# Performance work log

Measured on AMD Instinct MI355X. Metric: run time of the kernel, lower is better.

The kernel has to match this reference:

```python
import jax, jax.numpy as jnp
import numpy as np

T, D_IN, D_OUT = 8192, 1024, 1024
TRACE, CONTEXT = 64, 16


def setup_inputs() -> dict:
    key = jax.random.key(0)
    ks = jax.random.split(key, 8)
    x = jax.random.normal(ks[0], (T, D_IN), jnp.float32)
    state_re = jnp.zeros((1, TRACE, CONTEXT), jnp.float32)
    state_im = jnp.zeros((1, TRACE, CONTEXT), jnp.float32)
    start = jax.random.bernoulli(ks[1], 0.01, (T,))
    next_done = jax.random.bernoulli(ks[2], 0.01, (T,))
    lim_in = 1.0 / np.sqrt(D_IN)
    W_pre = jax.random.uniform(ks[3], (TRACE, D_IN), jnp.float32, -lim_in, lim_in)
    b_pre = jnp.zeros((TRACE,), jnp.float32)
    W_skip = jax.random.uniform(ks[4], (D_OUT, D_IN), jnp.float32, -lim_in, lim_in)
    b_skip = jnp.zeros((D_OUT,), jnp.float32)
    d_mix = 2 * TRACE * CONTEXT
    lim_mix = 1.0 / np.sqrt(d_mix)
    W_mix = jax.random.uniform(ks[5], (D_OUT, d_mix), jnp.float32, -lim_mix, lim_mix)
    b_mix = jnp.zeros((D_OUT,), jnp.float32)
    # ffa.init: deterministic decay rates a and oscillation freqs b (FFM paper)
    a = jnp.linspace(1e-6, 0.5, TRACE)
    b_freq = 2.0 * jnp.pi / jnp.linspace(1.0, 1024.0, CONTEXT)
    return dict(x=x, state_re=state_re, state_im=state_im, start=start, next_done=next_done,
                W_pre=W_pre, b_pre=b_pre, W_skip=W_skip, b_skip=b_skip,
                W_mix=W_mix, b_mix=b_mix, a=a, b_freq=b_freq)


def _ffa_scan(pre, state0, start, a, b_freq):
    """Resettable complex linear recurrence: S_t = gamma * S_{t-1} * !start_t + pre_t.
    pre: [T, m] real, state0: [1, m, c] complex. Returns [T, m, c] complex."""
    n = pre.shape[0]
    ab = (-jnp.abs(a)[:, None] + 1j * b_freq[None, :]).astype(jnp.complex64)  # [m, c]
    x_c = jnp.broadcast_to(pre[:, :, None], (n, pre.shape[1], b_freq.shape[0])).astype(jnp.complex64)
    # prepend carried-in state as an extra element with no decay (t=0) and no reset
    x_c = jnp.concatenate([state0, x_c], axis=0)
    s = jnp.concatenate([jnp.zeros((1,), bool), start.astype(bool)], axis=0)
    t = jnp.concatenate([jnp.zeros((1,), jnp.float32), jnp.ones((n,), jnp.float32)], axis=0)

    def combine(l, r):
        sl, xl, tl = l
        sr, xr, tr = r
        keep = jnp.logical_not(sr)  # right segment starts an episode -> drop left
        decay = jnp.exp(ab[None, :, :] * tr[:, None, None])  # gamma^{t_right}
        x = jnp.where(keep[:, None, None], xl * decay, jnp.zeros((), jnp.complex64)) + xr
        return (jnp.logical_or(sl, sr), x, tl * keep + tr)

    _, states, _ = jax.lax.associative_scan(combine, (s, x_c, t), axis=0)
    return states[1:]


def reference(x, state_re, state_im, start, next_done,
              W_pre, b_pre, W_skip, b_skip, W_mix, b_mix, a, b_freq):
    pre = x @ W_pre.T + b_pre                                  # [T, m]
    pre = pre / (1e-6 + jnp.linalg.norm(pre, axis=-1, keepdims=True))
    state0 = (state_re + 1j * state_im).astype(jnp.complex64)   # [1, m, c]
    states = _ffa_scan(pre, state0, start, a, b_freq)           # [T, m, c] complex
    z_in = jnp.concatenate([jnp.real(states), jnp.imag(states)], axis=-1)
    z_in = z_in.reshape(states.shape[0], -1)                    # [T, 2*m*c]
    z = z_in @ W_mix.T + b_mix                                  # [T, d_out]
    skip = x @ W_skip.T + b_skip                                # [T, d_out]
    return (z + skip, states[-1:])
```

## Files before the change

kernel.cpp:

```cpp
#include <hip/hip_runtime.h>
#include <hip/hip_bf16.h>
#include <stdint.h>

#define T_LEN 8192
#define DIN   1024
#define DOUT  1024
#define TRACE 64
#define CTX   16
#define KTOT  3072
#define CH    64
#define NCHUNK 128

#define AS1 __attribute__((address_space(1)))
#define AS3 __attribute__((address_space(3)))

#define BAR() asm volatile("s_barrier" ::: "memory")

using bf16 = __hip_bfloat16;
typedef __attribute__((ext_vector_type(4))) float f32x4;
typedef __attribute__((ext_vector_type(8))) short s16x8;

__device__ __forceinline__ void pack4(const float4 v, void* dst) {
    union { bf16 h[4]; uint2 u; } pk;
    pk.h[0] = __float2bfloat16(v.x); pk.h[1] = __float2bfloat16(v.y);
    pk.h[2] = __float2bfloat16(v.z); pk.h[3] = __float2bfloat16(v.w);
    *(uint2*)dst = pk.u;
}

__global__ void cvt_all(const float* __restrict__ x, const float* __restrict__ Wsk,
                        const float* __restrict__ Wmx, const float* __restrict__ Wpre,
                        bf16* __restrict__ A, bf16* __restrict__ Bc, bf16* __restrict__ Wp) {
    int idx = blockIdx.x * 256 + threadIdx.x;
    if (idx < 2097152) {
        int r = idx >> 8, c4 = (idx & 255) << 2;
        pack4(*(const float4*)(x + (size_t)r * 1024 + c4), A + (size_t)r * KTOT + c4);
    } else if (idx < 2359296) {
        int i = idx - 2097152;
        int r = i >> 8, c4 = (i & 255) << 2;
        pack4(*(const float4*)(Wsk + (size_t)r * 1024 + c4), Bc + (size_t)r * KTOT + c4);
    } else if (idx < 2883584) {
        int i = idx - 2359296;
        int r = i >> 9, c4 = (i & 511) << 2;
        pack4(*(const float4*)(Wmx + (size_t)r * 2048 + c4), Bc + (size_t)r * KTOT + 1024 + c4);
    } else if (idx < 2899968) {
        int i = idx - 2883584;
        int r = i >> 8, c4 = (i & 255) << 2;
        pack4(*(const float4*)(Wpre + (size_t)r * 1024 + c4), Wp + (size_t)r * 1024 + c4);
    }
}

__global__ __launch_bounds__(256) void pre_scan1(
    const bf16* __restrict__ A,
    const bf16* __restrict__ Wp,
    const float* __restrict__ bpre,
    const int* __restrict__ start,
    const float* __restrict__ a, const float* __restrict__ bfreq,
    float* __restrict__ pre_raw,
    float2* __restrict__ local_end,
    int* __restrict__ reset_any) {
    __shared__ short As[2][64 * 32];
    __shared__ short Bs[2][64 * 32];
    __shared__ float pn[CH][TRACE + 1];
    __shared__ float rn[CH];
    __shared__ int sf[CH];
    const int tid = threadIdx.x, lane = tid & 63, wv = tid >> 6;
    const int row0 = blockIdx.x * 64;
    const int l4 = lane >> 2, c8 = (lane & 3) * 8;

    auto stage = [&](int kt, int buf) {
        int r = wv * 16 + l4;
        const bf16* ga = A + (size_t)(row0 + r) * KTOT + kt * 32 + c8;
        const bf16* gb = Wp + (size_t)r * 1024 + kt * 32 + c8;
        __builtin_amdgcn_global_load_lds(
            (const AS1 void*)ga, (AS3 void*)&As[buf][wv * 512], 16, 0, 0);
        __builtin_amdgcn_global_load_lds(
            (const AS1 void*)gb, (AS3 void*)&Bs[buf][wv * 512], 16, 0, 0);
    };

    f32x4 acc[4];
#pragma unroll
    for (int j = 0; j < 4; ++j) acc[j] = (f32x4)0.0f;

    stage(0, 0);
    __syncthreads();
    int buf = 0;
    const int lr = lane & 15, lk = (lane >> 4) * 8;
    for (int kt = 0; kt < 32; ++kt) {
        if (kt + 1 < 32) stage(kt + 1, buf ^ 1);
        s16x8 af = *(const s16x8*)&As[buf][(wv * 16 + lr) * 32 + lk];
        s16x8 bfr[4];
#pragma unroll
        for (int j = 0; j < 4; ++j)
            bfr[j] = *(const s16x8*)&Bs[buf][(j * 16 + lr) * 32 + lk];
#pragma unroll
        for (int j = 0; j < 4; ++j)
            acc[j] = __builtin_amdgcn_mfma_f32_16x16x32_bf16(af, bfr[j], acc[j], 0, 0, 0);
        __syncthreads();
        buf ^= 1;
    }
    const int lg = lane >> 4;
#pragma unroll
    for (int j = 0; j < 4; ++j) {
        int col = j * 16 + lr;
        float bias = bpre[col];
#pragma unroll
        for (int r = 0; r < 4; ++r) {
            int rl = wv * 16 + lg * 4 + r;
            float v = acc[j][r] + bias;
            pn[rl][col] = v;
            pre_raw[(size_t)(row0 + rl) * TRACE + col] = v;
        }
    }
    if (tid < CH) sf[tid] = start[row0 + tid];
    __syncthreads();
    if (tid < CH) {
        float s = 0.f;
#pragma unroll
        for (int m = 0; m < TRACE; ++m) { float v = pn[tid][m]; s += v * v; }
        rn[tid] = 1.0f / (1e-6f + sqrtf(s));
        int any = __any(sf[tid] != 0);
        if (tid == 0) reset_any[blockIdx.x] = any;
    }
    __syncthreads();
#pragma unroll
    for (int q = 0; q < 4; ++q) {
        int pair = tid + q * 256;
        int m = pair >> 4, c = pair & 15;
        float am = a[m], th = bfreq[c];
        float e = expf(-fabsf(am));
        float sn, cs; sincosf(th, &sn, &cs);
        float gr = e * cs, gi = e * sn;
        float sre = 0.f, sim = 0.f;
        for (int r = 0; r < CH; ++r) {
            float p = pn[r][m] * rn[r];
            if (sf[r]) { sre = p; sim = 0.f; }
            else { float t = gr * sre - gi * sim + p; sim = gr * sim + gi * sre; sre = t; }
        }
        local_end[(size_t)blockIdx.x * 1024 + pair] = make_float2(sre, sim);
    }
}

__global__ void scan_phase2(const float2* __restrict__ local_end, const int* __restrict__ reset_any,
                            const float* __restrict__ state_re, const float* __restrict__ state_im,
                            const float* __restrict__ a, const float* __restrict__ bfreq,
                            float2* __restrict__ carry_in, float* __restrict__ out_tail, int tail_n) {
    const int pair = blockIdx.x * 64 + threadIdx.x;
    const int m = pair >> 4, c = pair & 15;
    float am = a[m], th = bfreq[c];
    float e = expf(-64.f * fabsf(am));
    float sn, cs; sincosf(64.f * th, &sn, &cs);
    float gr = e * cs, gi = e * sn;
    float cre = state_re[pair], cim = state_im[pair];

    float2 pf[8]; int rsv[8];
#pragma unroll
    for (int j = 0; j < 8; ++j) { pf[j] = local_end[(size_t)j * 1024 + pair]; rsv[j] = reset_any[j]; }
    for (int kb = 0; kb < NCHUNK; kb += 8) {
        float2 cur[8]; int rs[8];
#pragma unroll
        for (int j = 0; j < 8; ++j) { cur[j] = pf[j]; rs[j] = rsv[j]; }
        if (kb + 8 < NCHUNK) {
#pragma unroll
            for (int j = 0; j < 8; ++j) {
                pf[j]  = local_end[(size_t)(kb + 8 + j) * 1024 + pair];
                rsv[j] = reset_any[kb + 8 + j];
            }
        }
#pragma unroll
        for (int j = 0; j < 8; ++j) {
            carry_in[(size_t)(kb + j) * 1024 + pair] = make_float2(cre, cim);
            if (rs[j]) { cre = cur[j].x; cim = cur[j].y; }
            else {
                float t = gr * cre - gi * cim + cur[j].x;
                cim = gr * cim + gi * cre + cur[j].y;
                cre = t;
            }
        }
    }
    if (pair < tail_n)        out_tail[pair]        = cre;
    if (1024 + pair < tail_n) out_tail[1024 + pair] = cim;
}

__global__ void scan_phase3(const float* __restrict__ pre_raw, const int* __restrict__ start,
                            const float* __restrict__ a, const float* __restrict__ bfreq,
                            const float2* __restrict__ carry_in, bf16* __restrict__ A) {
    __shared__ float pn[CH][TRACE + 1];
    __shared__ float rn[CH];
    __shared__ int sf[CH];
    const int k = blockIdx.x, tid = threadIdx.x;
    for (int idx = tid; idx < CH * TRACE; idx += 256) {
        int r = idx >> 6, m = idx & 63;
        pn[r][m] = pre_raw[(size_t)(k * CH + r) * TRACE + m];
    }
    if (tid < CH) sf[tid] = start[k * CH + tid];
    __syncthreads();
    if (tid < CH) {
        float s = 0.f;
#pragma unroll
        for (int m = 0; m < TRACE; ++m) { float v = pn[tid][m]; s += v * v; }
        rn[tid] = 1.0f / (1e-6f + sqrtf(s));
    }
    __syncthreads();
#pragma unroll
    for (int q = 0; q < 2; ++q) {
        int p0 = q * 512 + tid * 2;
        int m = p0 >> 4, c0 = p0 & 15;
        float am = a[m];
        float e = expf(-fabsf(am));
        float sn0, cs0, sn1, cs1;
        sincosf(bfreq[c0], &sn0, &cs0);
        sincosf(bfreq[c0 + 1], &sn1, &cs1);
        float gr0 = e * cs0, gi0 = e * sn0;
        float gr1 = e * cs1, gi1 = e * sn1;
        float4 ci = *(const float4*)&carry_in[(size_t)k * 1024 + p0];
        float sre0 = ci.x, sim0 = ci.y, sre1 = ci.z, sim1 = ci.w;
        for (int r = 0; r < CH; ++r) {
            float p = pn[r][m] * rn[r];
            if (sf[r]) { sre0 = p; sim0 = 0.f; sre1 = p; sim1 = 0.f; }
            else {
                float t0 = gr0 * sre0 - gi0 * sim0 + p; sim0 = gr0 * sim0 + gi0 * sre0; sre0 = t0;
                float t1 = gr1 * sre1 - gi1 * sim1 + p; sim1 = gr1 * sim1 + gi1 * sre1; sre1 = t1;
            }
            size_t off = (size_t)(k * CH + r) * KTOT + 1024 + m * 32;
            union { bf16 h[2]; uint32_t u; } pr, pi;
            pr.h[0] = __float2bfloat16(sre0); pr.h[1] = __float2bfloat16(sre1);
            pi.h[0] = __float2bfloat16(sim0); pi.h[1] = __float2bfloat16(sim1);
            *(uint32_t*)(A + off + c0)      = pr.u;
            *(uint32_t*)(A + off + 16 + c0) = pi.u;
        }
    }
}

__global__ __launch_bounds__(512) void gemm_main(const bf16* __restrict__ A,
                                                 const bf16* __restrict__ B,
                                                 const float* __restrict__ bskip,
                                                 const float* __restrict__ bmix,
                                                 float* __restrict__ out) {
    __shared__ short As[3][256 * 64];
    __shared__ short Bs[3][128 * 64];
    const int tid = threadIdx.x;
    const int lane = tid & 63, wv = tid >> 6;
    const int wm = wv >> 1, wn = wv & 1;
    const int wg = blockIdx.x;
    const int xcd = wg & 7, bidx = wg >> 3;
    const int row0 = (xcd * 4 + (bidx >> 3)) * 256;
    const int col0 = (bidx & 7) * 128;

    const int rl8 = lane >> 3;
    const int u8  = lane & 7;
    const int ksw = (u8 ^ rl8) << 3;

    auto stageBatch = [&](int su, int bd, int sb) {
#pragma unroll
        for (int jj = 0; jj < 2; ++jj) {
            int j = sb * 2 + jj;
            int r = wv * 32 + j * 8 + rl8;
            const bf16* ga = A + (size_t)(row0 + r) * KTOT + su * 64 + ksw;
            __builtin_amdgcn_global_load_lds((const AS1 void*)ga,
                (AS3 void*)&As[bd][(wv * 32 + j * 8) * 64], 16, 0, 0);
        }
        int rb = wv * 16 + sb * 8 + rl8;
        const bf16* gb = B + (size_t)(col0 + rb) * KTOT + su * 64 + ksw;
        __builtin_amdgcn_global_load_lds((const AS1 void*)gb,
            (AS3 void*)&Bs[bd][(wv * 16 + sb * 8) * 64], 16, 0, 0);
    };

    f32x4 acc[4][4];
#pragma unroll
    for (int i = 0; i < 4; ++i)
#pragma unroll
        for (int j = 0; j < 4; ++j) acc[i][j] = (f32x4)0.0f;

    const int lr = lane & 15, hi = lane >> 4;
    const int sw0 = ((0 + hi) ^ (lr & 7)) << 3;
    const int sw1 = ((4 + hi) ^ (lr & 7)) << 3;

    s16x8 af[4][2], bfr[4][2];

    auto phase = [&](int bc, int h, int su, int bd, int vm) {
        if (h == 0) {
#pragma unroll
            for (int i = 0; i < 4; ++i) {
                af[i][0] = *(const s16x8*)&As[bc][(wm * 64 + i * 16 + lr) * 64 + sw0];
                af[i][1] = *(const s16x8*)&As[bc][(wm * 64 + i * 16 + lr) * 64 + sw1];
            }
#pragma unroll
            for (int j = 0; j < 2; ++j) {
                bfr[j][0] = *(const s16x8*)&Bs[bc][(wn * 64 + j * 16 + lr) * 64 + sw0];
                bfr[j][1] = *(const s16x8*)&Bs[bc][(wn * 64 + j * 16 + lr) * 64 + sw1];
            }
        } else {
#pragma unroll
            for (int j = 2; j < 4; ++j) {
                bfr[j][0] = *(const s16x8*)&Bs[bc][(wn * 64 + j * 16 + lr) * 64 + sw0];
                bfr[j][1] = *(const s16x8*)&Bs[bc][(wn * 64 + j * 16 + lr) * 64 + sw1];
            }
        }
        if (su >= 0) stageBatch(su, bd, h);
        BAR();
        __builtin_amdgcn_s_setprio(1);
#pragma unroll
        for (int kk = 0; kk < 2; ++kk)
#pragma unroll
            for (int i = 0; i < 4; ++i)
#pragma unroll
                for (int jj = 0; jj < 2; ++jj) {
                    int j = h * 2 + jj;
                    acc[i][j] = __builtin_amdgcn_mfma_f32_16x16x32_bf16(af[i][kk], bfr[j][kk], acc[i][j], 0, 0, 0);
                }
        __builtin_amdgcn_s_setprio(0);
        if (vm == 6)      asm volatile("s_waitcnt vmcnt(6)" ::: "memory");
        else if (vm == 0) asm volatile("s_waitcnt vmcnt(0)" ::: "memory");
        asm volatile("s_waitcnt lgkmcnt(0)" ::: "memory");
        BAR();
    };

    stageBatch(0, 0, 0); stageBatch(0, 0, 1);
    stageBatch(1, 1, 0); stageBatch(1, 1, 1);
    asm volatile("s_waitcnt vmcnt(6)" ::: "memory");
    BAR();

    for (int t = 0; t < 15; ++t) {
        int u0 = 3 * t;
        phase(0, 0, u0 + 2, 2, -1);
        phase(0, 1, u0 + 2, 2,  6);
        phase(1, 0, u0 + 3, 0, -1);
        phase(1, 1, u0 + 3, 0,  6);
        phase(2, 0, u0 + 4, 1, -1);
        phase(2, 1, u0 + 4, 1,  6);
    }
    phase(0, 0, 47, 2, -1);
    phase(0, 1, 47, 2,  6);
    phase(1, 0, -1, 0, -1);
    phase(1, 1, -1, 0,  0);
    phase(2, 0, -1, 0, -1);
    phase(2, 1, -1, 0, -1);

    const int lg = lane >> 4;
#pragma unroll
    for (int j = 0; j < 4; ++j) {
        int col = col0 + wn * 64 + j * 16 + lr;
        float bias = bskip[col] + bmix[col];
#pragma unroll
        for (int i = 0; i < 4; ++i) {
            int rbase = row0 + wm * 64 + i * 16 + lg * 4;
#pragma unroll
            for (int r = 0; r < 4; ++r)
                out[(size_t)(rbase + r) * DOUT + col] = acc[i][j][r] + bias;
        }
    }
}

extern "C" void kernel_launch(void* const* d_in, const int* in_sizes, int n_in,
                              void* d_out, int out_size, void* d_ws, size_t ws_size,
                              hipStream_t stream) {
    const float* x        = (const float*)d_in[0];
    const float* state_re = (const float*)d_in[1];
    const float* state_im = (const float*)d_in[2];
    const int*   start    = (const int*)d_in[3];
    const float* W_pre    = (const float*)d_in[5];
    const float* b_pre    = (const float*)d_in[6];
    const float* W_skip   = (const float*)d_in[7];
    const float* b_skip   = (const float*)d_in[8];
    const float* W_mix    = (const float*)d_in[9];
    const float* b_mix    = (const float*)d_in[10];
    const float* a_dec    = (const float*)d_in[11];
    const float* b_freq   = (const float*)d_in[12];

    uint8_t* ws = (uint8_t*)d_ws;
    bf16*  A         = (bf16*)(ws);
    bf16*  Bc        = (bf16*)(ws + 50331648);
    bf16*  Wp        = (bf16*)(ws + 56623104);
    float* pre_raw   = (float*)(ws + 56754176);
    float2* local_end= (float2*)(ws + 58851328);
    float2* carry_in = (float2*)(ws + 59899904);
    int*   reset_any = (int*)(ws + 60948480);

    cvt_all<<<dim3((2899968 + 255) / 256), 256, 0, stream>>>(x, W_skip, W_mix, W_pre, A, Bc, Wp);

    pre_scan1<<<dim3(NCHUNK), 256, 0, stream>>>(A, Wp, b_pre, start, a_dec, b_freq,
                                                pre_raw, local_end, reset_any);
    int tail_n = out_size - 8192 * 1024;
    if (tail_n < 0) tail_n = 0;
    if (tail_n > 2048) tail_n = 2048;
    scan_phase2<<<dim3(16), 64, 0, stream>>>(local_end, reset_any, state_re, state_im, a_dec, b_freq,
                                             carry_in, (float*)d_out + 8192 * 1024, tail_n);
    scan_phase3<<<dim3(NCHUNK), 256, 0, stream>>>(pre_raw, start, a_dec, b_freq, carry_in, A);

    gemm_main<<<dim3(256), 512, 0, stream>>>(A, Bc, b_skip, b_mix, (float*)d_out);
}
```

Baseline: 124.2 us.

## Split scan phase3 into half-size chunks using mid-chunk carries

Pre-scan now also records each 64-row chunk's local state at row 32, plus per-half reset flags. Phase2 uses these to derive carry-ins at 32-row granularity, applying a 32-step decay for the mid point. Phase3 then launches twice as many blocks, each with a 32-step sequential recurrence, to shorten its serial latency and raise occupancy. The cost is extra local_mid traffic and more work in the single-pass phase2.

```diff
diff --git a/kernel.cpp b/kernel.cpp
--- a/kernel.cpp
+++ b/kernel.cpp
@@ -9,7 +9,9 @@
 #define CTX   16
 #define KTOT  3072
 #define CH    64
+#define CH2   32
 #define NCHUNK 128
+#define NCHUNK2 256
 
 #define AS1 __attribute__((address_space(1)))
 #define AS3 __attribute__((address_space(3)))
@@ -57,7 +59,8 @@
     const float* __restrict__ a, const float* __restrict__ bfreq,
     float* __restrict__ pre_raw,
     float2* __restrict__ local_end,
-    int* __restrict__ reset_any) {
+    float2* __restrict__ local_mid,
+    int* __restrict__ ra0, int* __restrict__ ra1) {
     __shared__ short As[2][64 * 32];
     __shared__ short Bs[2][64 * 32];
     __shared__ float pn[CH][TRACE + 1];
@@ -118,8 +121,11 @@
 #pragma unroll
         for (int m = 0; m < TRACE; ++m) { float v = pn[tid][m]; s += v * v; }
         rn[tid] = 1.0f / (1e-6f + sqrtf(s));
-        int any = __any(sf[tid] != 0);
-        if (tid == 0) reset_any[blockIdx.x] = any;
+        unsigned long long b = __ballot(sf[tid] != 0);
+        if (tid == 0) {
+            ra0[blockIdx.x] = (b & 0xffffffffull) != 0;
+            ra1[blockIdx.x] = (b >> 32) != 0;
+        }
     }
     __syncthreads();
 #pragma unroll
@@ -135,44 +141,64 @@
             float p = pn[r][m] * rn[r];
             if (sf[r]) { sre = p; sim = 0.f; }
             else { float t = gr * sre - gi * sim + p; sim = gr * sim + gi * sre; sre = t; }
+            if (r == CH2 - 1)
+                local_mid[(size_t)blockIdx.x * 1024 + pair] = make_float2(sre, sim);
         }
         local_end[(size_t)blockIdx.x * 1024 + pair] = make_float2(sre, sim);
     }
 }
 
-__global__ void scan_phase2(const float2* __restrict__ local_end, const int* __restrict__ reset_any,
+__global__ void scan_phase2(const float2* __restrict__ local_end, const float2* __restrict__ local_mid,
+                            const int* __restrict__ ra0, const int* __restrict__ ra1,
                             const float* __restrict__ state_re, const float* __restrict__ state_im,
                             const float* __restrict__ a, const float* __restrict__ bfreq,
-                            float2* __restrict__ carry_in, float* __restrict__ out_tail, int tail_n) {
+                            float2* __restrict__ carry_in,
+                            float* __restrict__ out_tail, int tail_n) {
     const int pair = blockIdx.x * 64 + threadIdx.x;
     const int m = pair >> 4, c = pair & 15;
     float am = a[m], th = bfreq[c];
-    float e = expf(-64.f * fabsf(am));
-    float sn, cs; sincosf(64.f * th, &sn, &cs);
-    float gr = e * cs, gi = e * sn;
+    float e64 = expf(-64.f * fabsf(am));
+    float sn64, cs64; sincosf(64.f * th, &sn64, &cs64);
+    float gr64 = e64 * cs64, gi64 = e64 * sn64;
+    float e32 = expf(-32.f * fabsf(am));
+    float sn32, cs32; sincosf(32.f * th, &sn32, &cs32);
+    float gr32 = e32 * cs32, gi32 = e32 * sn32;
     float cre = state_re[pair], cim = state_im[pair];
 
-    float2 pf[8]; int rsv[8];
-#pragma unroll
-    for (int j = 0; j < 8; ++j) { pf[j] = local_end[(size_t)j * 1024 + pair]; rsv[j] = reset_any[j]; }
+    float2 pfE[8], pfM[8]; int pf0[8], pf1[8];
+#pragma unroll
+    for (int j = 0; j < 8; ++j) {
+        pfE[j] = local_end[(size_t)j * 1024 + pair];
+        pfM[j] = local_mid[(size_t)j * 1024 + pair];
+        pf0[j] = ra0[j]; pf1[j] = ra1[j];
+    }
     for (int kb = 0; kb < NCHUNK; kb += 8) {
-        float2 cur[8]; int rs[8];
-#pragma unroll
-        for (int j = 0; j < 8; ++j) { cur[j] = pf[j]; rs[j] = rsv[j]; }
+        float2 curE[8], curM[8]; int r0[8], r1[8];
+#pragma unroll
+        for (int j = 0; j < 8; ++j) { curE[j] = pfE[j]; curM[j] = pfM[j]; r0[j] = pf0[j]; r1[j] = pf1[j]; }
         if (kb + 8 < NCHUNK) {
 #pragma unroll
             for (int j = 0; j < 8; ++j) {
-                pf[j]  = local_end[(size_t)(kb + 8 + j) * 1024 + pair];
-                rsv[j] = reset_any[kb + 8 + j];
+                pfE[j] = local_end[(size_t)(kb + 8 + j) * 1024 + pair];
+                pfM[j] = local_mid[(size_t)(kb + 8 + j) * 1024 + pair];
+                pf0[j] = ra0[kb + 8 + j]; pf1[j] = ra1[kb + 8 + j];
             }
         }
 #pragma unroll
         for (int j = 0; j < 8; ++j) {
-            carry_in[(size_t)(kb + j) * 1024 + pair] = make_float2(cre, cim);
-            if (rs[j]) { cre = cur[j].x; cim = cur[j].y; }
+            int k = kb + j;
+            carry_in[(size_t)(2 * k) * 1024 + pair] = make_float2(cre, cim);
+            float hre, him;
+            if (r0[j]) { hre = curM[j].x; him = curM[j].y; }
             else {
-                float t = gr * cre - gi * cim + cur[j].x;
-                cim = gr * cim + gi * cre + cur[j].y;
+                hre = gr32 * cre - gi32 * cim + curM[j].x;
+                him = gr32 * cim + gi32 * cre + curM[j].y;
+            }
+            carry_in[(size_t)(2 * k + 1) * 1024 + pair] = make_float2(hre, him);
+            if (r0[j] | r1[j]) { cre = curE[j].x; cim = curE[j].y; }
+            else {
+                float t = gr64 * cre - gi64 * cim + curE[j].x;
+                cim = gr64 * cim + gi64 * cre + curE[j].y;
                 cre = t;
             }
         }
@@ -184,17 +210,18 @@
 __global__ void scan_phase3(const float* __restrict__ pre_raw, const int* __restrict__ start,
                             const float* __restrict__ a, const float* __restrict__ bfreq,
                             const float2* __restrict__ carry_in, bf16* __restrict__ A) {
-    __shared__ float pn[CH][TRACE + 1];
-    __shared__ float rn[CH];
-    __shared__ int sf[CH];
+    __shared__ float pn[CH2][TRACE + 1];
+    __shared__ float rn[CH2];
+    __shared__ int sf[CH2];
     const int k = blockIdx.x, tid = threadIdx.x;
-    for (int idx = tid; idx < CH * TRACE; idx += 256) {
+    const int rowb = k * CH2;
+    for (int idx = tid; idx < CH2 * TRACE; idx += 256) {
         int r = idx >> 6, m = idx & 63;
-        pn[r][m] = pre_raw[(size_t)(k * CH + r) * TRACE + m];
-    }
-    if (tid < CH) sf[tid] = start[k * CH + tid];
+        pn[r][m] = pre_raw[(size_t)(rowb + r) * TRACE + m];
+    }
+    if (tid < CH2) sf[tid] = start[rowb + tid];
     __syncthreads();
-    if (tid < CH) {
+    if (tid < CH2) {
         float s = 0.f;
 #pragma unroll
         for (int m = 0; m < TRACE; ++m) { float v = pn[tid][m]; s += v * v; }
@@ -214,14 +241,14 @@
         float gr1 = e * cs1, gi1 = e * sn1;
         float4 ci = *(const float4*)&carry_in[(size_t)k * 1024 + p0];
         float sre0 = ci.x, sim0 = ci.y, sre1 = ci.z, sim1 = ci.w;
-        for (int r = 0; r < CH; ++r) {
+        for (int r = 0; r < CH2; ++r) {
             float p = pn[r][m] * rn[r];
             if (sf[r]) { sre0 = p; sim0 = 0.f; sre1 = p; sim1 = 0.f; }
             else {
                 float t0 = gr0 * sre0 - gi0 * sim0 + p; sim0 = gr0 * sim0 + gi0 * sre0; sre0 = t0;
                 float t1 = gr1 * sre1 - gi1 * sim1 + p; sim1 = gr1 * sim1 + gi1 * sre1; sre1 = t1;
             }
-            size_t off = (size_t)(k * CH + r) * KTOT + 1024 + m * 32;
+            size_t off = (size_t)(rowb + r) * KTOT + 1024 + m * 32;
             union { bf16 h[2]; uint32_t u; } pr, pi;
             pr.h[0] = __float2bfloat16(sre0); pr.h[1] = __float2bfloat16(sre1);
             pi.h[0] = __float2bfloat16(sim0); pi.h[1] = __float2bfloat16(sim1);
@@ -373,19 +400,22 @@
     bf16*  Wp        = (bf16*)(ws + 56623104);
     float* pre_raw   = (float*)(ws + 56754176);
     float2* local_end= (float2*)(ws + 58851328);
-    float2* carry_in = (float2*)(ws + 59899904);
-    int*   reset_any = (int*)(ws + 60948480);
+    float2* local_mid= (float2*)(ws + 59899904);
+    float2* carry_in = (float2*)(ws + 60948480);
+    int*   ra0       = (int*)(ws + 63045632);
+    int*   ra1       = (int*)(ws + 63046656);
 
     cvt_all<<<dim3((2899968 + 255) / 256), 256, 0, stream>>>(x, W_skip, W_mix, W_pre, A, Bc, Wp);
 
     pre_scan1<<<dim3(NCHUNK), 256, 0, stream>>>(A, Wp, b_pre, start, a_dec, b_freq,
-                                                pre_raw, local_end, reset_any);
+                                                pre_raw, local_end, local_mid, ra0, ra1);
     int tail_n = out_size - 8192 * 1024;
     if (tail_n < 0) tail_n = 0;
     if (tail_n > 2048) tail_n = 2048;
-    scan_phase2<<<dim3(16), 64, 0, stream>>>(local_end, reset_any, state_re, state_im, a_dec, b_freq,
+    scan_phase2<<<dim3(16), 64, 0, stream>>>(local_end, local_mid, ra0, ra1,
+                                             state_re, state_im, a_dec, b_freq,
                                              carry_in, (float*)d_out + 8192 * 1024, tail_n);
-    scan_phase3<<<dim3(NCHUNK), 256, 0, stream>>>(pre_raw, start, a_dec, b_freq, carry_in, A);
+    scan_phase3<<<dim3(NCHUNK2), 256, 0, stream>>>(pre_raw, start, a_dec, b_freq, carry_in, A);
 
     gemm_main<<<dim3(256), 512, 0, stream>>>(A, Bc, b_skip, b_mix, (float*)d_out);
 }
```

Result: slower. 129.4 us (+4.2%).

## Fuse x bf16 conversion into pre-GEMM and overlap weight conversion with scan phase 2

Applied to the files above, without the earlier changes.

The x-to-bf16 conversion moves into pre_scan1, which loads fp32 x rows, packs them to bf16, writes them both to LDS for the MFMA and to the A buffer for the main GEMM. W_pre is now preloaded whole into LDS once per block. The W_skip/W_mix conversion is folded into the tiny scan_phase2 launch as extra blocks so it runs alongside the serial carry scan. This drops a separate pass over x and hides the weight conversion behind a latency-bound kernel, at the cost of a larger LDS footprint and extra barriers in pre_scan1.

```diff
diff --git a/kernel.cpp b/kernel.cpp
--- a/kernel.cpp
+++ b/kernel.cpp
@@ -10,6 +10,7 @@
 #define KTOT  3072
 #define CH    64
 #define NCHUNK 128
+#define WPLD  1032
 
 #define AS1 __attribute__((address_space(1)))
 #define AS3 __attribute__((address_space(3)))
@@ -27,75 +28,88 @@
     *(uint2*)dst = pk.u;
 }
 
-__global__ void cvt_all(const float* __restrict__ x, const float* __restrict__ Wsk,
-                        const float* __restrict__ Wmx, const float* __restrict__ Wpre,
-                        bf16* __restrict__ A, bf16* __restrict__ Bc, bf16* __restrict__ Wp) {
+__device__ __forceinline__ uint4 pack8(const float4 a, const float4 b) {
+    union { bf16 h[8]; uint4 u; } pk;
+    pk.h[0] = __float2bfloat16(a.x); pk.h[1] = __float2bfloat16(a.y);
+    pk.h[2] = __float2bfloat16(a.z); pk.h[3] = __float2bfloat16(a.w);
+    pk.h[4] = __float2bfloat16(b.x); pk.h[5] = __float2bfloat16(b.y);
+    pk.h[6] = __float2bfloat16(b.z); pk.h[7] = __float2bfloat16(b.w);
+    return pk.u;
+}
+
+__global__ void cvt_wp(const float* __restrict__ Wpre, bf16* __restrict__ Wp) {
     int idx = blockIdx.x * 256 + threadIdx.x;
-    if (idx < 2097152) {
-        int r = idx >> 8, c4 = (idx & 255) << 2;
-        pack4(*(const float4*)(x + (size_t)r * 1024 + c4), A + (size_t)r * KTOT + c4);
-    } else if (idx < 2359296) {
-        int i = idx - 2097152;
-        int r = i >> 8, c4 = (i & 255) << 2;
-        pack4(*(const float4*)(Wsk + (size_t)r * 1024 + c4), Bc + (size_t)r * KTOT + c4);
-    } else if (idx < 2883584) {
-        int i = idx - 2359296;
-        int r = i >> 9, c4 = (i & 511) << 2;
-        pack4(*(const float4*)(Wmx + (size_t)r * 2048 + c4), Bc + (size_t)r * KTOT + 1024 + c4);
-    } else if (idx < 2899968) {
-        int i = idx - 2883584;
-        int r = i >> 8, c4 = (i & 255) << 2;
-        pack4(*(const float4*)(Wpre + (size_t)r * 1024 + c4), Wp + (size_t)r * 1024 + c4);
-    }
+    int r = idx >> 8, c4 = (idx & 255) << 2;
+    pack4(*(const float4*)(Wpre + (size_t)r * 1024 + c4), Wp + (size_t)r * 1024 + c4);
 }
 
 __global__ __launch_bounds__(256) void pre_scan1(
-    const bf16* __restrict__ A,
+    const float* __restrict__ x,
     const bf16* __restrict__ Wp,
+    bf16* __restrict__ A,
     const float* __restrict__ bpre,
     const int* __restrict__ start,
     const float* __restrict__ a, const float* __restrict__ bfreq,
     float* __restrict__ pre_raw,
     float2* __restrict__ local_end,
     int* __restrict__ reset_any) {
+    __shared__ short Ws[64 * WPLD];
     __shared__ short As[2][64 * 32];
-    __shared__ short Bs[2][64 * 32];
     __shared__ float pn[CH][TRACE + 1];
     __shared__ float rn[CH];
     __shared__ int sf[CH];
     const int tid = threadIdx.x, lane = tid & 63, wv = tid >> 6;
     const int row0 = blockIdx.x * 64;
-    const int l4 = lane >> 2, c8 = (lane & 3) * 8;
-
-    auto stage = [&](int kt, int buf) {
-        int r = wv * 16 + l4;
-        const bf16* ga = A + (size_t)(row0 + r) * KTOT + kt * 32 + c8;
-        const bf16* gb = Wp + (size_t)r * 1024 + kt * 32 + c8;
-        __builtin_amdgcn_global_load_lds(
-            (const AS1 void*)ga, (AS3 void*)&As[buf][wv * 512], 16, 0, 0);
-        __builtin_amdgcn_global_load_lds(
-            (const AS1 void*)gb, (AS3 void*)&Bs[buf][wv * 512], 16, 0, 0);
-    };
+
+    for (int rr = 0; rr < 16; ++rr) {
+        int row = wv * 16 + rr;
+#pragma unroll
+        for (int h = 0; h < 2; ++h) {
+            const bf16* src = Wp + (size_t)row * 1024 + h * 512 + lane * 8;
+            __builtin_amdgcn_global_load_lds((const AS1 void*)src,
+                (AS3 void*)&Ws[row * WPLD + h * 512], 16, 0, 0);
+        }
+    }
+
+    const int r  = tid >> 2;
+    const int c0 = (tid & 3) * 8;
+    const float* xrow = x + (size_t)(row0 + r) * 1024;
+    bf16* arow = A + (size_t)(row0 + r) * KTOT;
 
     f32x4 acc[4];
 #pragma unroll
     for (int j = 0; j < 4; ++j) acc[j] = (f32x4)0.0f;
 
-    stage(0, 0);
-    __syncthreads();
+    float4 cur0 = *(const float4*)(xrow + c0);
+    float4 cur1 = *(const float4*)(xrow + c0 + 4);
+
+    asm volatile("s_waitcnt vmcnt(0)" ::: "memory");
+    BAR();
+
+    const int lr = lane & 15, lk = (lane >> 4) * 8;
     int buf = 0;
-    const int lr = lane & 15, lk = (lane >> 4) * 8;
     for (int kt = 0; kt < 32; ++kt) {
-        if (kt + 1 < 32) stage(kt + 1, buf ^ 1);
+        float4 nxt0, nxt1;
+        if (kt + 1 < 32) {
+            nxt0 = *(const float4*)(xrow + (kt + 1) * 32 + c0);
+            nxt1 = *(const float4*)(xrow + (kt + 1) * 32 + c0 + 4);
+        }
+        uint4 pk = pack8(cur0, cur1);
+        *(uint4*)&As[buf][r * 32 + c0] = pk;
+        *(uint4*)(arow + kt * 32 + c0) = pk;
+        asm volatile("s_waitcnt lgkmcnt(0)" ::: "memory");
+        BAR();
         s16x8 af = *(const s16x8*)&As[buf][(wv * 16 + lr) * 32 + lk];
         s16x8 bfr[4];
 #pragma unroll
         for (int j = 0; j < 4; ++j)
-            bfr[j] = *(const s16x8*)&Bs[buf][(j * 16 + lr) * 32 + lk];
+            bfr[j] = *(const s16x8*)&Ws[(j * 16 + lr) * WPLD + kt * 32 + lk];
 #pragma unroll
         for (int j = 0; j < 4; ++j)
             acc[j] = __builtin_amdgcn_mfma_f32_16x16x32_bf16(af, bfr[j], acc[j], 0, 0, 0);
-        __syncthreads();
+        asm volatile("s_waitcnt lgkmcnt(0)" ::: "memory");
+        BAR();
+        cur0 = nxt0; cur1 = nxt1;
         buf ^= 1;
     }
     const int lg = lane >> 4;
@@ -104,9 +118,9 @@
         int col = j * 16 + lr;
         float bias = bpre[col];
 #pragma unroll
-        for (int r = 0; r < 4; ++r) {
-            int rl = wv * 16 + lg * 4 + r;
-            float v = acc[j][r] + bias;
+        for (int q = 0; q < 4; ++q) {
+            int rl = wv * 16 + lg * 4 + q;
+            float v = acc[j][q] + bias;
             pn[rl][col] = v;
             pre_raw[(size_t)(row0 + rl) * TRACE + col] = v;
         }
@@ -131,19 +145,34 @@
         float sn, cs; sincosf(th, &sn, &cs);
         float gr = e * cs, gi = e * sn;
         float sre = 0.f, sim = 0.f;
-        for (int r = 0; r < CH; ++r) {
-            float p = pn[r][m] * rn[r];
-            if (sf[r]) { sre = p; sim = 0.f; }
+        for (int rr = 0; rr < CH; ++rr) {
+            float p = pn[rr][m] * rn[rr];
+            if (sf[rr]) { sre = p; sim = 0.f; }
             else { float t = gr * sre - gi * sim + p; sim = gr * sim + gi * sre; sre = t; }
         }
         local_end[(size_t)blockIdx.x * 1024 + pair] = make_float2(sre, sim);
     }
 }
 
-__global__ void scan_phase2(const float2* __restrict__ local_end, const int* __restrict__ reset_any,
-                            const float* __restrict__ state_re, const float* __restrict__ state_im,
-                            const float* __restrict__ a, const float* __restrict__ bfreq,
-                            float2* __restrict__ carry_in, float* __restrict__ out_tail, int tail_n) {
+__global__ void scan_phase2w(const float2* __restrict__ local_end, const int* __restrict__ reset_any,
+                             const float* __restrict__ state_re, const float* __restrict__ state_im,
+                             const float* __restrict__ a, const float* __restrict__ bfreq,
+                             float2* __restrict__ carry_in, float* __restrict__ out_tail, int tail_n,
+                             const float* __restrict__ Wsk, const float* __restrict__ Wmx,
+                             bf16* __restrict__ Bc) {
+    if (blockIdx.x >= 16) {
+        int idx = (blockIdx.x - 16) * 256 + threadIdx.x;
+        if (idx < 262144) {
+            int r = idx >> 8, c4 = (idx & 255) << 2;
+            pack4(*(const float4*)(Wsk + (size_t)r * 1024 + c4), Bc + (size_t)r * KTOT + c4);
+        } else {
+            int i = idx - 262144;
+            int r = i >> 9, c4 = (i & 511) << 2;
+            pack4(*(const float4*)(Wmx + (size_t)r * 2048 + c4), Bc + (size_t)r * KTOT + 1024 + c4);
+        }
+        return;
+    }
+    if (threadIdx.x >= 64) return;
     const int pair = blockIdx.x * 64 + threadIdx.x;
     const int m = pair >> 4, c = pair & 15;
     float am = a[m], th = bfreq[c];
@@ -376,15 +405,17 @@
     float2* carry_in = (float2*)(ws + 59899904);
     int*   reset_any = (int*)(ws + 60948480);
 
-    cvt_all<<<dim3((2899968 + 255) / 256), 256, 0, stream>>>(x, W_skip, W_mix, W_pre, A, Bc, Wp);
-
-    pre_scan1<<<dim3(NCHUNK), 256, 0, stream>>>(A, Wp, b_pre, start, a_dec, b_freq,
+    cvt_wp<<<dim3(64), 256, 0, stream>>>(W_pre, Wp);
+
+    pre_scan1<<<dim3(NCHUNK), 256, 0, stream>>>(x, Wp, A, b_pre, start, a_dec, b_freq,
                                                 pre_raw, local_end, reset_any);
     int tail_n = out_size - 8192 * 1024;
     if (tail_n < 0) tail_n = 0;
     if (tail_n > 2048) tail_n = 2048;
-    scan_phase2<<<dim3(16), 64, 0, stream>>>(local_end, reset_any, state_re, state_im, a_dec, b_freq,
-                                             carry_in, (float*)d_out + 8192 * 1024, tail_n);
+    scan_phase2w<<<dim3(16 + 3072), 256, 0, stream>>>(local_end, reset_any, state_re, state_im,
+                                                      a_dec, b_freq, carry_in,
+                                                      (float*)d_out + 8192 * 1024, tail_n,
+                                                      W_skip, W_mix, Bc);
     scan_phase3<<<dim3(NCHUNK), 256, 0, stream>>>(pre_raw, start, a_dec, b_freq, carry_in, A);
 
     gemm_main<<<dim3(256), 512, 0, stream>>>(A, Bc, b_skip, b_mix, (float*)d_out);
```

Result: slower. 133.4 us (+7.4%).
